# Optimization experiments

Measured on AMD Instinct MI355X. Metric: run time of the kernel, lower is better.

## Reference

```python
import jax, jax.numpy as jnp
import numpy as np

DIM = 384; HEADS = 6; K = 10; G = 2
GC = DIM // G            # group channel dim
HD = DIM // HEADS        # head dim
SCALE = HD ** -0.5
LN_EPS = 1e-5


def _sqdist(a, b):
    # a: [..., n, 3], b: [..., m, 3] -> [..., n, m]
    return (jnp.sum(a * a, -1)[..., :, None]
            + jnp.sum(b * b, -1)[..., None, :]
            - 2.0 * jnp.einsum('...nc,...mc->...nm', a, b))


def setup_inputs() -> dict:
    key = jax.random.key(0)
    ks = jax.random.split(key, 12)
    B, N, M = 4, 1024, 1024
    s = 0.02
    return {
        'q': jax.random.normal(ks[0], (B, N, DIM), jnp.float32),
        'q_pos': jax.random.normal(ks[1], (B, N, 3), jnp.float32),
        'v': jax.random.normal(ks[2], (B, M, DIM), jnp.float32),
        'v_pos': jax.random.normal(ks[3], (B, M, 3), jnp.float32),
        'Wq': jax.random.normal(ks[4], (DIM, DIM), jnp.float32) * s,
        'Wk': jax.random.normal(ks[5], (DIM, DIM), jnp.float32) * s,
        'Wv': jax.random.normal(ks[6], (DIM, DIM), jnp.float32) * s,
        'Wvoff': jax.random.normal(ks[7], (DIM, DIM), jnp.float32) * s,
        'Woff1': jax.random.normal(ks[8], (DIM, 2 * GC), jnp.float32) * s,
        'boff1': jnp.zeros((DIM,), jnp.float32),
        'ln_g': jnp.ones((DIM,), jnp.float32),
        'ln_b': jnp.zeros((DIM,), jnp.float32),
        'Woff2': jax.random.normal(ks[9], (3, DIM), jnp.float32) * s,
        'Wproj': jax.random.normal(ks[10], (DIM, DIM), jnp.float32) * s,
        'bproj': jnp.zeros((DIM,), jnp.float32),
    }


def reference(q, q_pos, v, v_pos, Wq, Wk, Wv, Wvoff, Woff1, boff1,
              ln_g, ln_b, Woff2, Wproj, bproj):
    B, N, C = q.shape
    M = v.shape[1]

    # --- knn_point: K nearest v_pos for each q_pos ---
    idx = jax.lax.top_k(-_sqdist(q_pos, v_pos), K)[1]        # [B,N,K]
    idx_flat = idx.reshape(B, N * K, 1)

    qp = q @ Wq.T                                            # [B,N,C]
    v_off = v @ Wvoff.T                                      # [B,M,C]

    # index_points gathers
    local_v = jnp.take_along_axis(v_off, idx_flat, axis=1).reshape(B, N, K, C)
    local_v_pos = jnp.take_along_axis(v_pos, idx_flat, axis=1).reshape(B, N, K, 3)

    # group split: 'b n k (g c) -> b g n k c'
    off_local_v = local_v.reshape(B, N, K, G, GC).transpose(0, 3, 1, 2, 4)  # [B,G,N,K,GC]
    group_q = qp.reshape(B, N, G, GC).transpose(0, 2, 1, 3)                 # [B,G,N,GC]

    shift_feat = jnp.concatenate(
        [off_local_v, jnp.broadcast_to(group_q[:, :, :, None, :], (B, G, N, K, GC))], -1)

    # linear_offset MLP: Linear -> LayerNorm -> GELU(exact) -> Linear, then tanh
    h = shift_feat @ Woff1.T + boff1                          # [B,G,N,K,DIM]
    mu = h.mean(-1, keepdims=True)
    var = h.var(-1, keepdims=True)
    h = (h - mu) / jnp.sqrt(var + LN_EPS) * ln_g + ln_b
    h = jax.nn.gelu(h, approximate=False)
    offset = jnp.tanh(h @ Woff2.T)                            # [B,G,N,K,3]

    shift_pos = (local_v_pos[:, None] + offset).reshape(B, G, N * K, 3)
    vg = v.reshape(B, M, G, GC).transpose(0, 2, 1, 3)         # [B,G,M,GC]

    # --- three_nn + reciprocal-distance three_interpolate ---
    sqd = _sqdist(shift_pos, v_pos[:, None])                  # [B,G,N*K,M]
    negd, idx3 = jax.lax.top_k(-sqd, 3)                       # 3 smallest
    dist = jnp.sqrt(jnp.maximum(-negd, 0.0))                  # [B,G,N*K,3]
    w = 1.0 / (dist + 1e-8)
    w = w / jnp.sum(w, -1, keepdims=True)
    feats = jnp.take_along_axis(vg, idx3.reshape(B, G, N * K * 3, 1), axis=2)
    feats = feats.reshape(B, G, N * K, 3, GC)
    interp = jnp.einsum('bgnj,bgnjc->bgnc', w, feats)         # [B,G,N*K,GC]
    # '(b g) (n k) c -> b n k (g c)'
    interp = interp.reshape(B, G, N, K, GC).transpose(0, 2, 3, 1, 4).reshape(B, N, K, C)

    # --- local cross-attention (each query attends to its K interpolated feats) ---
    kf = (interp @ Wk.T).reshape(B, N, K, HEADS, HD)
    vf = (interp @ Wv.T).reshape(B, N, K, HEADS, HD)
    qh = qp.reshape(B, N, HEADS, HD)
    attn = jnp.einsum('bnhd,bnkhd->bhnk', qh, kf) * SCALE
    attn = jax.nn.softmax(attn, axis=-1)
    out = jnp.einsum('bhnk,bnkhd->bnhd', attn, vf).reshape(B, N, C)
    return out @ Wproj.T + bproj
```

## Files before the change

kernel.cpp:

```cpp
#include <hip/hip_runtime.h>
#include <math.h>

#define NB 4
#define NN 1024
#define NM 1024
#define NC 384
#define NK 10
#define NG 2
#define NGC 192
#define NH 6

#define GSZ ((size_t)NB * NM * NC)
#define QSZ ((size_t)NB * NN * NC)
#define NCNC ((size_t)NC * NC)

#define OFF_WQ 0
#define OFF_W1B 147456
#define OFF_WK0 221184
#define OFF_WK1 294912
#define OFF_WV0 368640
#define OFF_WV1 442368
#define OFF_WPROJ 516096
#define WT_ALL_FLOATS 663552

__device__ __forceinline__ float wred_sum(float v) {
#pragma unroll
  for (int m = 32; m >= 1; m >>= 1) v += __shfl_xor(v, m, 64);
  return v;
}

__device__ __forceinline__ ushort f2bf(float x) {
  unsigned u = __float_as_uint(x);
  unsigned r = (u + 0x7fffu + ((u >> 16) & 1u)) >> 16;
  return (ushort)r;
}
__device__ __forceinline__ float b2f_lo(unsigned kv) {
  return __uint_as_float(kv << 16);
}
__device__ __forceinline__ float b2f_hi(unsigned kv) {
  return __uint_as_float(kv & 0xffff0000u);
}

__global__ void transpose_all_k(const float* __restrict__ Wq, const float* __restrict__ Woff1,
                                const float* __restrict__ Wk, const float* __restrict__ Wv,
                                const float* __restrict__ Wproj, float* __restrict__ Wt_all) {
  const float* W;
  int i0, icount, doff;
  switch (blockIdx.y) {
    case 0: W = Wq;    i0 = 0;   icount = NC;  doff = OFF_WQ;    break;
    case 1: W = Woff1; i0 = NGC; icount = NGC; doff = OFF_W1B;   break;
    case 2: W = Wk;    i0 = 0;   icount = NGC; doff = OFF_WK0;   break;
    case 3: W = Wk;    i0 = NGC; icount = NGC; doff = OFF_WK1;   break;
    case 4: W = Wv;    i0 = 0;   icount = NGC; doff = OFF_WV0;   break;
    case 5: W = Wv;    i0 = NGC; icount = NGC; doff = OFF_WV1;   break;
    default: W = Wproj; i0 = 0;  icount = NC;  doff = OFF_WPROJ; break;
  }
  int id = blockIdx.x * 256 + threadIdx.x;
  if (id >= icount * NC) return;
  int o = id % NC;
  int i = id / NC;
  Wt_all[doff + (size_t)i * NC + o] = W[(size_t)o * NC + i0 + i];
}

__global__ void wcomb_k(const float* __restrict__ Woff1, const float* __restrict__ Wvoff,
                        float* __restrict__ Wcomb_t) {
  int o = blockIdx.x;
  int g = blockIdx.y;
  int i = threadIdx.x;
  __shared__ float w1[NGC];
  if (i < NGC) w1[i] = Woff1[(size_t)o * NC + i];
  __syncthreads();
  float acc = 0.f;
#pragma unroll 4
  for (int j = 0; j < NGC; ++j)
    acc = fmaf(w1[j], Wvoff[(size_t)(g * NGC + j) * NC + i], acc);
  Wcomb_t[((size_t)g * NC + i) * NC + o] = acc;
}

__global__ __launch_bounds__(384) void gemm16_k(const float* __restrict__ X, int IN, int xoff0,
                                                int xoff_stride, const float* __restrict__ Wt0,
                                                size_t wstride, const float* __restrict__ bias,
                                                float* __restrict__ Y0, size_t ystride) {
  __shared__ __align__(16) float xs[NC][20];
  int tid = threadIdx.x;
  int og = tid % 96, rg = tid / 96;
  int r0 = blockIdx.x * 16;
  int job = blockIdx.y;
  int xoff = xoff0 + job * xoff_stride;
  const float* Wt = Wt0 + (size_t)job * wstride;
  float* Y = Y0 + (size_t)job * ystride;
  for (int t = tid; t < 16 * IN; t += 384) {
    int r = t / IN, kk = t % IN;
    xs[kk][r] = X[(size_t)(r0 + r) * NC + xoff + kk];
  }
  __syncthreads();
  float acc[4][4];
#pragma unroll
  for (int i = 0; i < 4; ++i)
#pragma unroll
    for (int j = 0; j < 4; ++j) acc[i][j] = 0.f;
  int o = og * 4;
#pragma unroll 4
  for (int kk = 0; kk < IN; ++kk) {
    float4 w4 = *(const float4*)&Wt[(size_t)kk * NC + o];
    float4 x4 = *(const float4*)&xs[kk][rg * 4];
    float xr[4] = {x4.x, x4.y, x4.z, x4.w};
    float wr[4] = {w4.x, w4.y, w4.z, w4.w};
#pragma unroll
    for (int ri = 0; ri < 4; ++ri)
#pragma unroll
      for (int oi = 0; oi < 4; ++oi) acc[ri][oi] = fmaf(xr[ri], wr[oi], acc[ri][oi]);
  }
  float4 bv = make_float4(0.f, 0.f, 0.f, 0.f);
  if (bias) bv = *(const float4*)&bias[o];
#pragma unroll
  for (int ri = 0; ri < 4; ++ri) {
    float4 ov;
    ov.x = acc[ri][0] + bv.x;
    ov.y = acc[ri][1] + bv.y;
    ov.z = acc[ri][2] + bv.z;
    ov.w = acc[ri][3] + bv.w;
    *(float4*)&Y[(size_t)(r0 + rg * 4 + ri) * NC + o] = ov;
  }
}

__global__ __launch_bounds__(384) void vproj_k(const float* __restrict__ v,
                                               const float* __restrict__ Wcomb_t,
                                               const float* __restrict__ Wt_all,
                                               float* __restrict__ vcontrib,
                                               unsigned* __restrict__ KVc) {
  __shared__ __align__(16) float xs[NC][20];
  int tid = threadIdx.x;
  int og = tid % 96, rg = tid / 96;
  int r0 = blockIdx.x * 16;
  int job = blockIdx.y;
  int o = og * 4;
  if (job < 2) {
    const float* Wt = job ? (Wcomb_t + NCNC) : Wcomb_t;
    float* Yf = job ? (vcontrib + GSZ) : vcontrib;
    for (int t = tid; t < 16 * NC; t += 384) {
      int r = t / NC, kk = t % NC;
      xs[kk][r] = v[(size_t)(r0 + r) * NC + kk];
    }
    __syncthreads();
    float acc[4][4];
#pragma unroll
    for (int i = 0; i < 4; ++i)
#pragma unroll
      for (int j = 0; j < 4; ++j) acc[i][j] = 0.f;
#pragma unroll 4
    for (int kk = 0; kk < NC; ++kk) {
      float4 w4 = *(const float4*)&Wt[(size_t)kk * NC + o];
      float4 x4 = *(const float4*)&xs[kk][rg * 4];
      float xr[4] = {x4.x, x4.y, x4.z, x4.w};
      float wr[4] = {w4.x, w4.y, w4.z, w4.w};
#pragma unroll
      for (int ri = 0; ri < 4; ++ri)
#pragma unroll
        for (int oi = 0; oi < 4; ++oi) acc[ri][oi] = fmaf(xr[ri], wr[oi], acc[ri][oi]);
    }
#pragma unroll
    for (int ri = 0; ri < 4; ++ri)
      *(float4*)&Yf[(size_t)(r0 + rg * 4 + ri) * NC + o] =
          make_float4(acc[ri][0], acc[ri][1], acc[ri][2], acc[ri][3]);
  } else {
    int g = job - 2;
    int xoff = g * NGC;
    const float* WtK = Wt_all + (g ? OFF_WK1 : OFF_WK0);
    const float* WtV = Wt_all + (g ? OFF_WV1 : OFF_WV0);
    unsigned* Yu = KVc + (size_t)g * GSZ;
    for (int t = tid; t < 16 * NGC; t += 384) {
      int r = t / NGC, kk = t % NGC;
      xs[kk][r] = v[(size_t)(r0 + r) * NC + xoff + kk];
    }
    __syncthreads();
    float aK[4][4], aV[4][4];
#pragma unroll
    for (int i = 0; i < 4; ++i)
#pragma unroll
      for (int j = 0; j < 4; ++j) { aK[i][j] = 0.f; aV[i][j] = 0.f; }
#pragma unroll 2
    for (int kk = 0; kk < NGC; ++kk) {
      float4 wk = *(const float4*)&WtK[(size_t)kk * NC + o];
      float4 wv = *(const float4*)&WtV[(size_t)kk * NC + o];
      float4 x4 = *(const float4*)&xs[kk][rg * 4];
      float xr[4] = {x4.x, x4.y, x4.z, x4.w};
      float wkr[4] = {wk.x, wk.y, wk.z, wk.w};
      float wvr[4] = {wv.x, wv.y, wv.z, wv.w};
#pragma unroll
      for (int ri = 0; ri < 4; ++ri)
#pragma unroll
        for (int oi = 0; oi < 4; ++oi) {
          aK[ri][oi] = fmaf(xr[ri], wkr[oi], aK[ri][oi]);
          aV[ri][oi] = fmaf(xr[ri], wvr[oi], aV[ri][oi]);
        }
    }
#pragma unroll
    for (int ri = 0; ri < 4; ++ri) {
      uint4 pk;
      pk.x = (unsigned)f2bf(aK[ri][0]) | ((unsigned)f2bf(aV[ri][0]) << 16);
      pk.y = (unsigned)f2bf(aK[ri][1]) | ((unsigned)f2bf(aV[ri][1]) << 16);
      pk.z = (unsigned)f2bf(aK[ri][2]) | ((unsigned)f2bf(aV[ri][2]) << 16);
      pk.w = (unsigned)f2bf(aK[ri][3]) | ((unsigned)f2bf(aV[ri][3]) << 16);
      *(uint4*)&Yu[(size_t)(r0 + rg * 4 + ri) * NC + o] = pk;
    }
  }
}

__global__ __launch_bounds__(256) void knn2_k(const float* __restrict__ q_pos,
                                              const float* __restrict__ v_pos,
                                              int* __restrict__ knn_idx) {
  __shared__ float4 cpos[NM];
  int tid = threadIdx.x, lane = tid & 63, wid = tid >> 6;
  int b = blockIdx.x / (NN / 4);
  int n = (blockIdx.x % (NN / 4)) * 4 + wid;
  for (int t = tid; t < NM; t += 256) {
    float x = v_pos[((size_t)b * NM + t) * 3 + 0];
    float y = v_pos[((size_t)b * NM + t) * 3 + 1];
    float z = v_pos[((size_t)b * NM + t) * 3 + 2];
    cpos[t] = make_float4(x, y, z, x * x + y * y + z * z);
  }
  __syncthreads();
  float qx = q_pos[((size_t)b * NN + n) * 3 + 0];
  float qy = q_pos[((size_t)b * NN + n) * 3 + 1];
  float qz = q_pos[((size_t)b * NN + n) * 3 + 2];
  float qq = qx * qx + qy * qy + qz * qz;
  float bd[NK];
  int bi[NK];
#pragma unroll
  for (int j = 0; j < NK; ++j) { bd[j] = 1e30f; bi[j] = 0x7fffffff; }
#pragma unroll
  for (int t = 0; t < NM / 64; ++t) {
    int m = t * 64 + lane;
    float4 cc = cpos[m];
    float d = qq + cc.w - 2.f * (qx * cc.x + qy * cc.y + qz * cc.z);
    if (d < bd[NK - 1]) {
#pragma unroll
      for (int j = NK - 1; j > 0; --j) {
        if (d < bd[j - 1]) { bd[j] = bd[j - 1]; bi[j] = bi[j - 1]; }
        else if (d < bd[j]) { bd[j] = d; bi[j] = m; }
      }
      if (d < bd[0]) { bd[0] = d; bi[0] = m; }
    }
  }
  size_t base = ((size_t)b * NN + n) * NK;
#pragma unroll
  for (int round = 0; round < NK; ++round) {
    float dh = bd[0];
    int mh = bi[0];
#pragma unroll
    for (int off = 32; off >= 1; off >>= 1) {
      float od = __shfl_xor(dh, off, 64);
      int om = __shfl_xor(mh, off, 64);
      if (od < dh || (od == dh && om < mh)) { dh = od; mh = om; }
    }
    if (lane == 0) knn_idx[base + round] = mh;
    if (bi[0] == mh) {
#pragma unroll
      for (int j = 0; j < NK - 1; ++j) { bd[j] = bd[j + 1]; bi[j] = bi[j + 1]; }
      bd[NK - 1] = 1e30f; bi[NK - 1] = 0x7fffffff;
    }
  }
}

__global__ __launch_bounds__(256) void mlp3nn_k(
    const float* __restrict__ vcontrib, const float* __restrict__ qcontrib,
    const float* __restrict__ boff1, const float* __restrict__ ln_g,
    const float* __restrict__ ln_b, const float* __restrict__ Woff2,
    const int* __restrict__ knn_idx, const float* __restrict__ v_pos,
    int* __restrict__ idx3, float* __restrict__ w3) {
  __shared__ float4 cpos[NM];
  int tid = threadIdx.x, lane = tid & 63, wid = tid >> 6;
  int ra = blockIdx.x * 8 + wid * 2;
  int rb = ra + 1;
  int b = (blockIdx.x * 8) / (NK * NN * NG);
  for (int t = tid; t < NM; t += 256) {
    float x = v_pos[((size_t)b * NM + t) * 3 + 0];
    float y = v_pos[((size_t)b * NM + t) * 3 + 1];
    float z = v_pos[((size_t)b * NM + t) * 3 + 2];
    cpos[t] = make_float4(x, y, z, x * x + y * y + z * z);
  }
  __syncthreads();
  int ka = ra % NK;
  int na = (ra / NK) % NN;
  int ga = (ra / (NK * NN)) % NG;
  int ma = knn_idx[((size_t)b * NN + na) * NK + ka];
  int mb = knn_idx[((size_t)b * NN + na) * NK + ka + 1];
  const float* vca = vcontrib + ((size_t)(ga * NB + b) * NM + ma) * NC;
  const float* vcb = vcontrib + ((size_t)(ga * NB + b) * NM + mb) * NC;
  const float* qca = qcontrib + ((size_t)(ga * NB + b) * NN + na) * NC;
  float ha[6], hb[6];
  float sa = 0.f, s2a = 0.f, sb = 0.f, s2b = 0.f;
#pragma unroll
  for (int j = 0; j < 6; ++j) {
    int c = j * 64 + lane;
    float qj = qca[c];
    float bo = boff1[c];
    float xa = vca[c] + qj + bo;
    float xb = vcb[c] + qj + bo;
    ha[j] = xa; sa += xa; s2a += xa * xa;
    hb[j] = xb; sb += xb; s2b += xb * xb;
  }
#pragma unroll
  for (int off = 32; off >= 1; off >>= 1) {
    sa += __shfl_xor(sa, off, 64);
    s2a += __shfl_xor(s2a, off, 64);
    sb += __shfl_xor(sb, off, 64);
    s2b += __shfl_xor(s2b, off, 64);
  }
  float meana = sa * (1.f / NC), meanb = sb * (1.f / NC);
  float vara = s2a * (1.f / NC) - meana * meana;
  float varb = s2b * (1.f / NC) - meanb * meanb;
  float inva = 1.f / sqrtf(vara + 1e-5f);
  float invb = 1.f / sqrtf(varb + 1e-5f);
  float p0a = 0.f, p1a = 0.f, p2a = 0.f, p0b = 0.f, p1b = 0.f, p2b = 0.f;
#pragma unroll
  for (int j = 0; j < 6; ++j) {
    int c = j * 64 + lane;
    float gg = ln_g[c], bb = ln_b[c];
    float w0 = Woff2[0 * NC + c], w1 = Woff2[1 * NC + c], w2 = Woff2[2 * NC + c];
    float xa = (ha[j] - meana) * inva * gg + bb;
    xa = 0.5f * xa * (1.f + erff(xa * 0.70710678118654752f));
    float xb = (hb[j] - meanb) * invb * gg + bb;
    xb = 0.5f * xb * (1.f + erff(xb * 0.70710678118654752f));
    p0a = fmaf(xa, w0, p0a); p1a = fmaf(xa, w1, p1a); p2a = fmaf(xa, w2, p2a);
    p0b = fmaf(xb, w0, p0b); p1b = fmaf(xb, w1, p1b); p2b = fmaf(xb, w2, p2b);
  }
#pragma unroll
  for (int off = 32; off >= 1; off >>= 1) {
    p0a += __shfl_xor(p0a, off, 64);
    p1a += __shfl_xor(p1a, off, 64);
    p2a += __shfl_xor(p2a, off, 64);
    p0b += __shfl_xor(p0b, off, 64);
    p1b += __shfl_xor(p1b, off, 64);
    p2b += __shfl_xor(p2b, off, 64);
  }
  float4 cma = cpos[ma], cmb = cpos[mb];
  float sxa = cma.x + tanhf(p0a), sya = cma.y + tanhf(p1a), sza = cma.z + tanhf(p2a);
  float sxb = cmb.x + tanhf(p0b), syb = cmb.y + tanhf(p1b), szb = cmb.z + tanhf(p2b);
  float qqa = sxa * sxa + sya * sya + sza * sza;
  float qqb = sxb * sxb + syb * syb + szb * szb;
  float d0a = 1e30f, d1a = 1e30f, d2a = 1e30f;
  float d0b = 1e30f, d1b = 1e30f, d2b = 1e30f;
  int i0a = 0x7fffffff, i1a = 0x7fffffff, i2a = 0x7fffffff;
  int i0b = 0x7fffffff, i1b = 0x7fffffff, i2b = 0x7fffffff;
#pragma unroll 4
  for (int t = 0; t < NM / 64; ++t) {
    int m2 = t * 64 + lane;
    float4 cc = cpos[m2];
    float da = qqa + cc.w - 2.f * (sxa * cc.x + sya * cc.y + sza * cc.z);
    float db = qqb + cc.w - 2.f * (sxb * cc.x + syb * cc.y + szb * cc.z);
    float nd0a = fminf(da, d0a);
    float nd1a = __builtin_amdgcn_fmed3f(da, d0a, d1a);
    float nd2a = __builtin_amdgcn_fmed3f(da, d1a, d2a);
    i2a = (da < d1a) ? i1a : ((da < d2a) ? m2 : i2a);
    i1a = (da < d0a) ? i0a : ((da < d1a) ? m2 : i1a);
    i0a = (da < d0a) ? m2 : i0a;
    d0a = nd0a; d1a = nd1a; d2a = nd2a;
    float nd0b = fminf(db, d0b);
    float nd1b = __builtin_amdgcn_fmed3f(db, d0b, d1b);
    float nd2b = __builtin_amdgcn_fmed3f(db, d1b, d2b);
    i2b = (db < d1b) ? i1b : ((db < d2b) ? m2 : i2b);
    i1b = (db < d0b) ? i0b : ((db < d1b) ? m2 : i1b);
    i0b = (db < d0b) ? m2 : i0b;
    d0b = nd0b; d1b = nd1b; d2b = nd2b;
  }
  float rda[3], rdb[3];
  int rma[3], rmb[3];
#pragma unroll
  for (int round = 0; round < 3; ++round) {
    float dha = d0a; int mha = i0a;
    float dhb = d0b; int mhb = i0b;
#pragma unroll
    for (int off = 32; off >= 1; off >>= 1) {
      float oda = __shfl_xor(dha, off, 64); int oma = __shfl_xor(mha, off, 64);
      float odb = __shfl_xor(dhb, off, 64); int omb = __shfl_xor(mhb, off, 64);
      if (oda < dha || (oda == dha && oma < mha)) { dha = oda; mha = oma; }
      if (odb < dhb || (odb == dhb && omb < mhb)) { dhb = odb; mhb = omb; }
    }
    rda[round] = dha; rma[round] = mha;
    rdb[round] = dhb; rmb[round] = mhb;
    if (i0a == mha) { d0a = d1a; i0a = i1a; d1a = d2a; i1a = i2a; d2a = 1e30f; i2a = 0x7fffffff; }
    if (i0b == mhb) { d0b = d1b; i0b = i1b; d1b = d2b; i1b = i2b; d2b = 1e30f; i2b = 0x7fffffff; }
  }
  if (lane == 0) {
    float e0 = 1.f / (sqrtf(fmaxf(rda[0], 0.f)) + 1e-8f);
    float e1 = 1.f / (sqrtf(fmaxf(rda[1], 0.f)) + 1e-8f);
    float e2 = 1.f / (sqrtf(fmaxf(rda[2], 0.f)) + 1e-8f);
    float sw = e0 + e1 + e2;
    idx3[(size_t)ra * 3 + 0] = rma[0]; w3[(size_t)ra * 3 + 0] = e0 / sw;
    idx3[(size_t)ra * 3 + 1] = rma[1]; w3[(size_t)ra * 3 + 1] = e1 / sw;
    idx3[(size_t)ra * 3 + 2] = rma[2]; w3[(size_t)ra * 3 + 2] = e2 / sw;
    float f0 = 1.f / (sqrtf(fmaxf(rdb[0], 0.f)) + 1e-8f);
    float f1 = 1.f / (sqrtf(fmaxf(rdb[1], 0.f)) + 1e-8f);
    float f2 = 1.f / (sqrtf(fmaxf(rdb[2], 0.f)) + 1e-8f);
    float sw2 = f0 + f1 + f2;
    idx3[(size_t)rb * 3 + 0] = rmb[0]; w3[(size_t)rb * 3 + 0] = f0 / sw2;
    idx3[(size_t)rb * 3 + 1] = rmb[1]; w3[(size_t)rb * 3 + 1] = f1 / sw2;
    idx3[(size_t)rb * 3 + 2] = rmb[2]; w3[(size_t)rb * 3 + 2] = f2 / sw2;
  }
}

__global__ __launch_bounds__(NC) void attn_k(const float* __restrict__ qp,
                                             const unsigned* __restrict__ KV,
                                             const int* __restrict__ idx3,
                                             const float* __restrict__ w3,
                                             float* __restrict__ attn_out) {
  __shared__ float vfs[NK][NC];
  __shared__ float lgs[NH][NK];
  __shared__ int il[NG][NK][3];
  __shared__ float wl[NG][NK][3];
  int o = threadIdx.x;
  int lane = o & 63, wid = o >> 6;
  int b = blockIdx.x / NN;
  int n = blockIdx.x % NN;
  if (o < NG * NK * 3) {
    int g = o / (NK * 3), k = (o / 3) % NK, j = o % 3;
    size_t rr = (((size_t)(b * NG + g) * NN + n) * NK + k) * 3 + j;
    il[g][k][j] = idx3[rr];
    wl[g][k][j] = w3[rr];
  }
  __syncthreads();
  float qv = qp[((size_t)b * NN + n) * NC + o];
  for (int k = 0; k < NK; ++k) {
    float kf = 0.f, vf = 0.f;
#pragma unroll
    for (int g = 0; g < NG; ++g)
#pragma unroll
      for (int j = 0; j < 3; ++j) {
        int m = il[g][k][j];
        float w = wl[g][k][j];
        unsigned kv = KV[((size_t)(g * NB + b) * NM + m) * NC + o];
        kf = fmaf(w, b2f_lo(kv), kf);
        vf = fmaf(w, b2f_hi(kv), vf);
      }
    vfs[k][o] = vf;
    float p = wred_sum(qv * kf);
    if (lane == 0) lgs[wid][k] = p * 0.125f;
  }
  __syncthreads();
  float a[NK];
  float mx = -1e30f;
#pragma unroll
  for (int k = 0; k < NK; ++k) { a[k] = lgs[wid][k]; mx = fmaxf(mx, a[k]); }
  float sum = 0.f;
#pragma unroll
  for (int k = 0; k < NK; ++k) { a[k] = expf(a[k] - mx); sum += a[k]; }
  float outv = 0.f;
#pragma unroll
  for (int k = 0; k < NK; ++k) outv = fmaf(a[k] / sum, vfs[k][o], outv);
  attn_out[((size_t)b * NN + n) * NC + o] = outv;
}

extern "C" void kernel_launch(void* const* d_in, const int* in_sizes, int n_in,
                              void* d_out, int out_size, void* d_ws, size_t ws_size,
                              hipStream_t stream) {
  (void)in_sizes; (void)n_in; (void)out_size; (void)ws_size;
  const float* q     = (const float*)d_in[0];
  const float* q_pos = (const float*)d_in[1];
  const float* v     = (const float*)d_in[2];
  const float* v_pos = (const float*)d_in[3];
  const float* Wq    = (const float*)d_in[4];
  const float* Wk    = (const float*)d_in[5];
  const float* Wv    = (const float*)d_in[6];
  const float* Wvoff = (const float*)d_in[7];
  const float* Woff1 = (const float*)d_in[8];
  const float* boff1 = (const float*)d_in[9];
  const float* ln_g  = (const float*)d_in[10];
  const float* ln_b  = (const float*)d_in[11];
  const float* Woff2 = (const float*)d_in[12];
  const float* Wproj = (const float*)d_in[13];
  const float* bproj = (const float*)d_in[14];
  float* out = (float*)d_out;

  char* p = (char*)d_ws;
  auto alloc_f = [&](size_t n) { float* r = (float*)p; p += n * sizeof(float); return r; };
  auto alloc_u = [&](size_t n) { unsigned* r = (unsigned*)p; p += n * sizeof(unsigned); return r; };
  auto alloc_i = [&](size_t n) { int* r = (int*)p; p += n * sizeof(int); return r; };

  float* qp        = alloc_f(QSZ);
  float* qcontrib  = alloc_f((size_t)NG * QSZ);
  float* vcontrib  = alloc_f((size_t)NG * GSZ);
  float* Wt_all    = alloc_f((size_t)WT_ALL_FLOATS);
  float* Wcomb_t   = alloc_f((size_t)NG * NCNC);
  float* w3        = alloc_f((size_t)NB * NG * NN * NK * 3);
  unsigned* KVc    = alloc_u((size_t)NG * GSZ);
  int* knn_idx     = alloc_i((size_t)NB * NN * NK);
  int* idx3        = alloc_i((size_t)NB * NG * NN * NK * 3);
  float* attn_out  = vcontrib;

  transpose_all_k<<<dim3(576, 7), 256, 0, stream>>>(Wq, Woff1, Wk, Wv, Wproj, Wt_all);
  wcomb_k<<<dim3(NC, NG), NC, 0, stream>>>(Woff1, Wvoff, Wcomb_t);

  gemm16_k<<<dim3(NB * NN / 16, 1), 384, 0, stream>>>(q, NC, 0, 0, Wt_all + OFF_WQ, 0, nullptr,
                                                      qp, 0);
  knn2_k<<<NB * (NN / 4), 256, 0, stream>>>(q_pos, v_pos, knn_idx);
  gemm16_k<<<dim3(NB * NN / 16, 2), 384, 0, stream>>>(qp, NGC, 0, NGC, Wt_all + OFF_W1B, 0,
                                                      nullptr, qcontrib, QSZ);
  vproj_k<<<dim3(NB * NM / 16, 4), 384, 0, stream>>>(v, Wcomb_t, Wt_all, vcontrib, KVc);

  mlp3nn_k<<<NB * NG * NN * NK / 8, 256, 0, stream>>>(vcontrib, qcontrib, boff1, ln_g, ln_b,
                                                      Woff2, knn_idx, v_pos, idx3, w3);
  attn_k<<<NB * NN, NC, 0, stream>>>(qp, KVc, idx3, w3, attn_out);
  gemm16_k<<<dim3(NB * NN / 16, 1), 384, 0, stream>>>(attn_out, NC, 0, 0, Wt_all + OFF_WPROJ, 0,
                                                      bproj, out, 0);
}
```

Measured before the change: 463.2 us.

## Merge weight prep kernels and fuse front projections with kNN into one launch

Merges the weight transpose and the combined-weight GEMM into a single prep kernel. Packs the q projection, v projections (offset, K/V) and the kNN search into one multi-job front kernel indexed by blockIdx.y. This cuts launch count and lets independent front-end work share the GPU at the same time. In exchange the grid has idle blocks (684 blocks per job where GEMM jobs need only 256), and the combined-weight path now reads Woff1 from global memory without shared-memory staging.

```diff
diff --git a/kernel.cpp b/kernel.cpp
--- a/kernel.cpp
+++ b/kernel.cpp
@@ -41,40 +41,188 @@
   return __uint_as_float(kv & 0xffff0000u);
 }
 
-__global__ void transpose_all_k(const float* __restrict__ Wq, const float* __restrict__ Woff1,
-                                const float* __restrict__ Wk, const float* __restrict__ Wv,
-                                const float* __restrict__ Wproj, float* __restrict__ Wt_all) {
-  const float* W;
-  int i0, icount, doff;
-  switch (blockIdx.y) {
-    case 0: W = Wq;    i0 = 0;   icount = NC;  doff = OFF_WQ;    break;
-    case 1: W = Woff1; i0 = NGC; icount = NGC; doff = OFF_W1B;   break;
-    case 2: W = Wk;    i0 = 0;   icount = NGC; doff = OFF_WK0;   break;
-    case 3: W = Wk;    i0 = NGC; icount = NGC; doff = OFF_WK1;   break;
-    case 4: W = Wv;    i0 = 0;   icount = NGC; doff = OFF_WV0;   break;
-    case 5: W = Wv;    i0 = NGC; icount = NGC; doff = OFF_WV1;   break;
-    default: W = Wproj; i0 = 0;  icount = NC;  doff = OFF_WPROJ; break;
-  }
+__global__ __launch_bounds__(256) void prep_k(const float* __restrict__ Wq,
+                                              const float* __restrict__ Woff1,
+                                              const float* __restrict__ Wk,
+                                              const float* __restrict__ Wv,
+                                              const float* __restrict__ Wproj,
+                                              const float* __restrict__ Wvoff,
+                                              float* __restrict__ Wt_all,
+                                              float* __restrict__ Wcomb_t) {
+  int job = blockIdx.y;
   int id = blockIdx.x * 256 + threadIdx.x;
-  if (id >= icount * NC) return;
-  int o = id % NC;
-  int i = id / NC;
-  Wt_all[doff + (size_t)i * NC + o] = W[(size_t)o * NC + i0 + i];
-}
-
-__global__ void wcomb_k(const float* __restrict__ Woff1, const float* __restrict__ Wvoff,
-                        float* __restrict__ Wcomb_t) {
-  int o = blockIdx.x;
-  int g = blockIdx.y;
-  int i = threadIdx.x;
-  __shared__ float w1[NGC];
-  if (i < NGC) w1[i] = Woff1[(size_t)o * NC + i];
-  __syncthreads();
-  float acc = 0.f;
+  if (job < 7) {
+    const float* W;
+    int i0, icount, doff;
+    switch (job) {
+      case 0: W = Wq;    i0 = 0;   icount = NC;  doff = OFF_WQ;    break;
+      case 1: W = Woff1; i0 = NGC; icount = NGC; doff = OFF_W1B;   break;
+      case 2: W = Wk;    i0 = 0;   icount = NGC; doff = OFF_WK0;   break;
+      case 3: W = Wk;    i0 = NGC; icount = NGC; doff = OFF_WK1;   break;
+      case 4: W = Wv;    i0 = 0;   icount = NGC; doff = OFF_WV0;   break;
+      case 5: W = Wv;    i0 = NGC; icount = NGC; doff = OFF_WV1;   break;
+      default: W = Wproj; i0 = 0;  icount = NC;  doff = OFF_WPROJ; break;
+    }
+    if (id >= icount * NC) return;
+    int o = id % NC;
+    int i = id / NC;
+    Wt_all[doff + (size_t)i * NC + o] = W[(size_t)o * NC + i0 + i];
+  } else {
+    int g = job - 7;
+    int o = id % NC;
+    int i = id / NC;
+    float acc = 0.f;
 #pragma unroll 4
-  for (int j = 0; j < NGC; ++j)
-    acc = fmaf(w1[j], Wvoff[(size_t)(g * NGC + j) * NC + i], acc);
-  Wcomb_t[((size_t)g * NC + i) * NC + o] = acc;
+    for (int j = 0; j < NGC; ++j)
+      acc = fmaf(Woff1[(size_t)o * NC + j], Wvoff[(size_t)(g * NGC + j) * NC + i], acc);
+    Wcomb_t[((size_t)(g * NC + i)) * NC + o] = acc;
+  }
+}
+
+__global__ __launch_bounds__(384) void front_k(const float* __restrict__ q,
+                                               const float* __restrict__ v,
+                                               const float* __restrict__ q_pos,
+                                               const float* __restrict__ v_pos,
+                                               const float* __restrict__ Wcomb_t,
+                                               const float* __restrict__ Wt_all,
+                                               float* __restrict__ qp,
+                                               float* __restrict__ vcontrib,
+                                               unsigned* __restrict__ KVc,
+                                               int* __restrict__ knn_idx) {
+  __shared__ __align__(16) float xs[NC][20];
+  int tid = threadIdx.x;
+  int job = blockIdx.y;
+  if (job == 5) {
+    float4* cpos = (float4*)&xs[0][0];
+    int lane = tid & 63, wid = tid >> 6;
+    int bx = blockIdx.x;
+    int b = bx / 171;
+    int n = (bx % 171) * 6 + wid;
+    for (int t = tid; t < NM; t += 384) {
+      float x = v_pos[((size_t)b * NM + t) * 3 + 0];
+      float y = v_pos[((size_t)b * NM + t) * 3 + 1];
+      float z = v_pos[((size_t)b * NM + t) * 3 + 2];
+      cpos[t] = make_float4(x, y, z, x * x + y * y + z * z);
+    }
+    __syncthreads();
+    if (n >= NN) return;
+    float qx = q_pos[((size_t)b * NN + n) * 3 + 0];
+    float qy = q_pos[((size_t)b * NN + n) * 3 + 1];
+    float qz = q_pos[((size_t)b * NN + n) * 3 + 2];
+    float qq = qx * qx + qy * qy + qz * qz;
+    float bd[NK];
+    int bi[NK];
+#pragma unroll
+    for (int j = 0; j < NK; ++j) { bd[j] = 1e30f; bi[j] = 0x7fffffff; }
+#pragma unroll
+    for (int t = 0; t < NM / 64; ++t) {
+      int m = t * 64 + lane;
+      float4 cc = cpos[m];
+      float d = qq + cc.w - 2.f * (qx * cc.x + qy * cc.y + qz * cc.z);
+      if (d < bd[NK - 1]) {
+#pragma unroll
+        for (int j = NK - 1; j > 0; --j) {
+          if (d < bd[j - 1]) { bd[j] = bd[j - 1]; bi[j] = bi[j - 1]; }
+          else if (d < bd[j]) { bd[j] = d; bi[j] = m; }
+        }
+        if (d < bd[0]) { bd[0] = d; bi[0] = m; }
+      }
+    }
+    size_t base = ((size_t)b * NN + n) * NK;
+#pragma unroll
+    for (int round = 0; round < NK; ++round) {
+      float dh = bd[0];
+      int mh = bi[0];
+#pragma unroll
+      for (int off = 32; off >= 1; off >>= 1) {
+        float od = __shfl_xor(dh, off, 64);
+        int om = __shfl_xor(mh, off, 64);
+        if (od < dh || (od == dh && om < mh)) { dh = od; mh = om; }
+      }
+      if (lane == 0) knn_idx[base + round] = mh;
+      if (bi[0] == mh) {
+#pragma unroll
+        for (int j = 0; j < NK - 1; ++j) { bd[j] = bd[j + 1]; bi[j] = bi[j + 1]; }
+        bd[NK - 1] = 1e30f; bi[NK - 1] = 0x7fffffff;
+      }
+    }
+    return;
+  }
+  if (blockIdx.x >= 256) return;
+  int og = tid % 96, rg = tid / 96;
+  int r0 = blockIdx.x * 16;
+  int o = og * 4;
+  if (job == 2 || job == 3) {
+    int g = job - 2;
+    int xoff = g * NGC;
+    const float* WtK = Wt_all + (g ? OFF_WK1 : OFF_WK0);
+    const float* WtV = Wt_all + (g ? OFF_WV1 : OFF_WV0);
+    unsigned* Yu = KVc + (size_t)g * GSZ;
+    for (int t = tid; t < 16 * NGC; t += 384) {
+      int r = t / NGC, kk = t % NGC;
+      xs[kk][r] = v[(size_t)(r0 + r) * NC + xoff + kk];
+    }
+    __syncthreads();
+    float aK[4][4], aV[4][4];
+#pragma unroll
+    for (int i = 0; i < 4; ++i)
+#pragma unroll
+      for (int j = 0; j < 4; ++j) { aK[i][j] = 0.f; aV[i][j] = 0.f; }
+#pragma unroll 2
+    for (int kk = 0; kk < NGC; ++kk) {
+      float4 wk = *(const float4*)&WtK[(size_t)kk * NC + o];
+      float4 wv = *(const float4*)&WtV[(size_t)kk * NC + o];
+      float4 x4 = *(const float4*)&xs[kk][rg * 4];
+      float xr[4] = {x4.x, x4.y, x4.z, x4.w};
+      float wkr[4] = {wk.x, wk.y, wk.z, wk.w};
+      float wvr[4] = {wv.x, wv.y, wv.z, wv.w};
+#pragma unroll
+      for (int ri = 0; ri < 4; ++ri)
+#pragma unroll
+        for (int oi = 0; oi < 4; ++oi) {
+          aK[ri][oi] = fmaf(xr[ri], wkr[oi], aK[ri][oi]);
+          aV[ri][oi] = fmaf(xr[ri], wvr[oi], aV[ri][oi]);
+        }
+    }
+#pragma unroll
+    for (int ri = 0; ri < 4; ++ri) {
+      uint4 pk;
+      pk.x = (unsigned)f2bf(aK[ri][0]) | ((unsigned)f2bf(aV[ri][0]) << 16);
+      pk.y = (unsigned)f2bf(aK[ri][1]) | ((unsigned)f2bf(aV[ri][1]) << 16);
+      pk.z = (unsigned)f2bf(aK[ri][2]) | ((unsigned)f2bf(aV[ri][2]) << 16);
+      pk.w = (unsigned)f2bf(aK[ri][3]) | ((unsigned)f2bf(aV[ri][3]) << 16);
+      *(uint4*)&Yu[(size_t)(r0 + rg * 4 + ri) * NC + o] = pk;
+    }
+  } else {
+    const float* X = (job == 4) ? q : v;
+    const float* Wt = (job == 0) ? Wcomb_t : (job == 1) ? (Wcomb_t + NCNC) : (Wt_all + OFF_WQ);
+    float* Yf = (job == 0) ? vcontrib : (job == 1) ? (vcontrib + GSZ) : qp;
+    for (int t = tid; t < 16 * NC; t += 384) {
+      int r = t / NC, kk = t % NC;
+      xs[kk][r] = X[(size_t)(r0 + r) * NC + kk];
+    }
+    __syncthreads();
+    float acc[4][4];
+#pragma unroll
+    for (int i = 0; i < 4; ++i)
+#pragma unroll
+      for (int j = 0; j < 4; ++j) acc[i][j] = 0.f;
+#pragma unroll 4
+    for (int kk = 0; kk < NC; ++kk) {
+      float4 w4 = *(const float4*)&Wt[(size_t)kk * NC + o];
+      float4 x4 = *(const float4*)&xs[kk][rg * 4];
+      float xr[4] = {x4.x, x4.y, x4.z, x4.w};
+      float wr[4] = {w4.x, w4.y, w4.z, w4.w};
+#pragma unroll
+      for (int ri = 0; ri < 4; ++ri)
+#pragma unroll
+        for (int oi = 0; oi < 4; ++oi) acc[ri][oi] = fmaf(xr[ri], wr[oi], acc[ri][oi]);
+    }
+#pragma unroll
+    for (int ri = 0; ri < 4; ++ri)
+      *(float4*)&Yf[(size_t)(r0 + rg * 4 + ri) * NC + o] =
+          make_float4(acc[ri][0], acc[ri][1], acc[ri][2], acc[ri][3]);
+  }
 }
 
 __global__ __launch_bounds__(384) void gemm16_k(const float* __restrict__ X, int IN, int xoff0,
@@ -121,145 +269,6 @@
     ov.z = acc[ri][2] + bv.z;
     ov.w = acc[ri][3] + bv.w;
     *(float4*)&Y[(size_t)(r0 + rg * 4 + ri) * NC + o] = ov;
-  }
-}
-
-__global__ __launch_bounds__(384) void vproj_k(const float* __restrict__ v,
-                                               const float* __restrict__ Wcomb_t,
-                                               const float* __restrict__ Wt_all,
-                                               float* __restrict__ vcontrib,
-                                               unsigned* __restrict__ KVc) {
-  __shared__ __align__(16) float xs[NC][20];
-  int tid = threadIdx.x;
-  int og = tid % 96, rg = tid / 96;
-  int r0 = blockIdx.x * 16;
-  int job = blockIdx.y;
-  int o = og * 4;
-  if (job < 2) {
-    const float* Wt = job ? (Wcomb_t + NCNC) : Wcomb_t;
-    float* Yf = job ? (vcontrib + GSZ) : vcontrib;
-    for (int t = tid; t < 16 * NC; t += 384) {
-      int r = t / NC, kk = t % NC;
-      xs[kk][r] = v[(size_t)(r0 + r) * NC + kk];
-    }
-    __syncthreads();
-    float acc[4][4];
-#pragma unroll
-    for (int i = 0; i < 4; ++i)
-#pragma unroll
-      for (int j = 0; j < 4; ++j) acc[i][j] = 0.f;
-#pragma unroll 4
-    for (int kk = 0; kk < NC; ++kk) {
-      float4 w4 = *(const float4*)&Wt[(size_t)kk * NC + o];
-      float4 x4 = *(const float4*)&xs[kk][rg * 4];
-      float xr[4] = {x4.x, x4.y, x4.z, x4.w};
-      float wr[4] = {w4.x, w4.y, w4.z, w4.w};
-#pragma unroll
-      for (int ri = 0; ri < 4; ++ri)
-#pragma unroll
-        for (int oi = 0; oi < 4; ++oi) acc[ri][oi] = fmaf(xr[ri], wr[oi], acc[ri][oi]);
-    }
-#pragma unroll
-    for (int ri = 0; ri < 4; ++ri)
-      *(float4*)&Yf[(size_t)(r0 + rg * 4 + ri) * NC + o] =
-          make_float4(acc[ri][0], acc[ri][1], acc[ri][2], acc[ri][3]);
-  } else {
-    int g = job - 2;
-    int xoff = g * NGC;
-    const float* WtK = Wt_all + (g ? OFF_WK1 : OFF_WK0);
-    const float* WtV = Wt_all + (g ? OFF_WV1 : OFF_WV0);
-    unsigned* Yu = KVc + (size_t)g * GSZ;
-    for (int t = tid; t < 16 * NGC; t += 384) {
-      int r = t / NGC, kk = t % NGC;
-      xs[kk][r] = v[(size_t)(r0 + r) * NC + xoff + kk];
-    }
-    __syncthreads();
-    float aK[4][4], aV[4][4];
-#pragma unroll
-    for (int i = 0; i < 4; ++i)
-#pragma unroll
-      for (int j = 0; j < 4; ++j) { aK[i][j] = 0.f; aV[i][j] = 0.f; }
-#pragma unroll 2
-    for (int kk = 0; kk < NGC; ++kk) {
-      float4 wk = *(const float4*)&WtK[(size_t)kk * NC + o];
-      float4 wv = *(const float4*)&WtV[(size_t)kk * NC + o];
-      float4 x4 = *(const float4*)&xs[kk][rg * 4];
-      float xr[4] = {x4.x, x4.y, x4.z, x4.w};
-      float wkr[4] = {wk.x, wk.y, wk.z, wk.w};
-      float wvr[4] = {wv.x, wv.y, wv.z, wv.w};
-#pragma unroll
-      for (int ri = 0; ri < 4; ++ri)
-#pragma unroll
-        for (int oi = 0; oi < 4; ++oi) {
-          aK[ri][oi] = fmaf(xr[ri], wkr[oi], aK[ri][oi]);
-          aV[ri][oi] = fmaf(xr[ri], wvr[oi], aV[ri][oi]);
-        }
-    }
-#pragma unroll
-    for (int ri = 0; ri < 4; ++ri) {
-      uint4 pk;
-      pk.x = (unsigned)f2bf(aK[ri][0]) | ((unsigned)f2bf(aV[ri][0]) << 16);
-      pk.y = (unsigned)f2bf(aK[ri][1]) | ((unsigned)f2bf(aV[ri][1]) << 16);
-      pk.z = (unsigned)f2bf(aK[ri][2]) | ((unsigned)f2bf(aV[ri][2]) << 16);
-      pk.w = (unsigned)f2bf(aK[ri][3]) | ((unsigned)f2bf(aV[ri][3]) << 16);
-      *(uint4*)&Yu[(size_t)(r0 + rg * 4 + ri) * NC + o] = pk;
-    }
-  }
-}
-
-__global__ __launch_bounds__(256) void knn2_k(const float* __restrict__ q_pos,
-                                              const float* __restrict__ v_pos,
-                                              int* __restrict__ knn_idx) {
-  __shared__ float4 cpos[NM];
-  int tid = threadIdx.x, lane = tid & 63, wid = tid >> 6;
-  int b = blockIdx.x / (NN / 4);
-  int n = (blockIdx.x % (NN / 4)) * 4 + wid;
-  for (int t = tid; t < NM; t += 256) {
-    float x = v_pos[((size_t)b * NM + t) * 3 + 0];
-    float y = v_pos[((size_t)b * NM + t) * 3 + 1];
-    float z = v_pos[((size_t)b * NM + t) * 3 + 2];
-    cpos[t] = make_float4(x, y, z, x * x + y * y + z * z);
-  }
-  __syncthreads();
-  float qx = q_pos[((size_t)b * NN + n) * 3 + 0];
-  float qy = q_pos[((size_t)b * NN + n) * 3 + 1];
-  float qz = q_pos[((size_t)b * NN + n) * 3 + 2];
-  float qq = qx * qx + qy * qy + qz * qz;
-  float bd[NK];
-  int bi[NK];
-#pragma unroll
-  for (int j = 0; j < NK; ++j) { bd[j] = 1e30f; bi[j] = 0x7fffffff; }
-#pragma unroll
-  for (int t = 0; t < NM / 64; ++t) {
-    int m = t * 64 + lane;
-    float4 cc = cpos[m];
-    float d = qq + cc.w - 2.f * (qx * cc.x + qy * cc.y + qz * cc.z);
-    if (d < bd[NK - 1]) {
-#pragma unroll
-      for (int j = NK - 1; j > 0; --j) {
-        if (d < bd[j - 1]) { bd[j] = bd[j - 1]; bi[j] = bi[j - 1]; }
-        else if (d < bd[j]) { bd[j] = d; bi[j] = m; }
-      }
-      if (d < bd[0]) { bd[0] = d; bi[0] = m; }
-    }
-  }
-  size_t base = ((size_t)b * NN + n) * NK;
-#pragma unroll
-  for (int round = 0; round < NK; ++round) {
-    float dh = bd[0];
-    int mh = bi[0];
-#pragma unroll
-    for (int off = 32; off >= 1; off >>= 1) {
-      float od = __shfl_xor(dh, off, 64);
-      int om = __shfl_xor(mh, off, 64);
-      if (od < dh || (od == dh && om < mh)) { dh = od; mh = om; }
-    }
-    if (lane == 0) knn_idx[base + round] = mh;
-    if (bi[0] == mh) {
-#pragma unroll
-      for (int j = 0; j < NK - 1; ++j) { bd[j] = bd[j + 1]; bi[j] = bi[j + 1]; }
-      bd[NK - 1] = 1e30f; bi[NK - 1] = 0x7fffffff;
-    }
   }
 }
 
@@ -489,16 +498,11 @@
   int* idx3        = alloc_i((size_t)NB * NG * NN * NK * 3);
   float* attn_out  = vcontrib;
 
-  transpose_all_k<<<dim3(576, 7), 256, 0, stream>>>(Wq, Woff1, Wk, Wv, Wproj, Wt_all);
-  wcomb_k<<<dim3(NC, NG), NC, 0, stream>>>(Woff1, Wvoff, Wcomb_t);
-
-  gemm16_k<<<dim3(NB * NN / 16, 1), 384, 0, stream>>>(q, NC, 0, 0, Wt_all + OFF_WQ, 0, nullptr,
-                                                      qp, 0);
-  knn2_k<<<NB * (NN / 4), 256, 0, stream>>>(q_pos, v_pos, knn_idx);
+  prep_k<<<dim3(576, 9), 256, 0, stream>>>(Wq, Woff1, Wk, Wv, Wproj, Wvoff, Wt_all, Wcomb_t);
+  front_k<<<dim3(684, 6), 384, 0, stream>>>(q, v, q_pos, v_pos, Wcomb_t, Wt_all, qp, vcontrib,
+                                            KVc, knn_idx);
   gemm16_k<<<dim3(NB * NN / 16, 2), 384, 0, stream>>>(qp, NGC, 0, NGC, Wt_all + OFF_W1B, 0,
                                                       nullptr, qcontrib, QSZ);
-  vproj_k<<<dim3(NB * NM / 16, 4), 384, 0, stream>>>(v, Wcomb_t, Wt_all, vcontrib, KVc);
-
   mlp3nn_k<<<NB * NG * NN * NK / 8, 256, 0, stream>>>(vcontrib, qcontrib, boff1, ln_g, ln_b,
                                                       Woff2, knn_idx, v_pos, idx3, w3);
   attn_k<<<NB * NN, NC, 0, stream>>>(qp, KVc, idx3, w3, attn_out);
```

Measured after the change: 493.5 us. 6.5% more time.
